# Performance work log

Measured on AMD Instinct MI355X. Metric: run time of the kernel, lower is better.

Reference implementation:

```python
import jax, jax.numpy as jnp
import numpy as np
from jax import lax
jax.config.update("jax_enable_x64", True)

B, N, H = 64, 2048, 64
FS, FC, C = 1.0e10, 3.0e11, 3.0e8
N_LAYERS, CG_STEPS = 4, 5
F32 = jnp.float32
_T64 = jnp.arange(N, dtype=jnp.float64) / FS  # time grid, float64 (FIX 7)


def _gru_dir(xproj, whh, bhh, reverse):
    # xproj: [B,N,3H] = x @ Wih^T + bih precomputed; torch gate order (r,z,n)
    def step(h, xp):
        gh = h @ whh.T + bhh
        r = jax.nn.sigmoid(xp[:, :H] + gh[:, :H])
        z = jax.nn.sigmoid(xp[:, H:2 * H] + gh[:, H:2 * H])
        n = jnp.tanh(xp[:, 2 * H:] + r * gh[:, 2 * H:])
        h2 = (1.0 - z) * n + z * h
        return h2, h2
    xs = jnp.swapaxes(xproj, 0, 1)
    if reverse:
        xs = xs[::-1]
    h0 = jnp.zeros((xproj.shape[0], H), xproj.dtype)
    _, hs = lax.scan(step, h0, xs)
    if reverse:
        hs = hs[::-1]
    return jnp.swapaxes(hs, 0, 1)


def _channel_diag(theta, bussgang_gain):
    # float64 phase: tau = R/c (single trip), phase = 2*pi*fc*(tau + (v/c)t + 0.5(a/c)t^2)
    th = theta.astype(jnp.float64)
    tau = th[:, 0:1] / C
    td = th[:, 1:2] / C
    tdd = th[:, 2:3] / C
    t = _T64[None, :]
    phase = 2.0 * np.pi * FC * (tau + td * t + 0.5 * tdd * t ** 2)
    h = jnp.exp(-1j * phase).astype(jnp.complex64)
    return h * bussgang_gain


def _forward(y_real, y_imag, theta, meta_features, gamma_eff, scale_slope, bussgang_gain,
             reg_w1, reg_b1, reg_w2, reg_b2, pw1, pb1, ln_g, ln_b, pw2, pb2, pw3, pb3,
             gru_wih_f, gru_whh_f, gru_bih_f, gru_bhh_f, gru_wih_b, gru_whh_b, gru_bih_b, gru_bhh_b,
             hw1, hb1, hw2, hb2, phase_bias):
    y_q = lax.complex(y_real, y_imag)
    # PhysicsEncoder.get_approx_fim_info
    reg = jax.nn.softplus(jax.nn.relu(gamma_eff @ reg_w1.T + reg_b1) @ reg_w2.T + reg_b2) + 1e-6  # [B,1]
    log_vol = -jnp.log(reg) * 3.0
    # PilotNavigator
    h1 = meta_features @ pw1.T + pb1
    mu = jnp.mean(h1, -1, keepdims=True)
    var = jnp.var(h1, -1, keepdims=True)
    h1 = (h1 - mu) / jnp.sqrt(var + 1e-5) * ln_g + ln_b
    h2 = jax.nn.relu(jax.nn.relu(h1) @ pw2.T + pb2)
    logits = h2 @ pw3.T + pb3
    g_PN = jax.nn.sigmoid(logits[:, 0:1])
    g_NL = jax.nn.softplus(logits[:, 1:2]) + 0.5
    physics_brake = jax.nn.sigmoid((log_vol - (-15.0)) * 5.0)
    g_grad = jax.nn.sigmoid(logits[:, 2:3]) * physics_brake
    # diagonal channel
    h_eff = _channel_diag(theta, bussgang_gain)  # [B,N] c64
    hh = (jnp.conj(h_eff) * h_eff).real  # |h|^2, [B,N]
    lam = reg  # damping from reg_net
    feats_raw = jnp.stack([y_q.real, y_q.imag], -1)  # [B,N,2]
    bias = lax.complex(jnp.cos(phase_bias), -jnp.sin(phase_bias))  # exp(-j*phase_bias)
    x_est = jnp.zeros((B, N), jnp.complex64)
    for _ in range(N_LAYERS):  # shared weights across layers
        # RiemannianPNTracker
        reliable = jnp.mean(jnp.abs(x_est)) > 0.1
        x_norm = x_est / (jnp.abs(x_est) + 1e-6)
        resid = y_q * jnp.conj(x_norm)
        feats = jnp.where(reliable, jnp.stack([resid.real, resid.imag], -1), feats_raw)
        xp_f = feats @ gru_wih_f.T + gru_bih_f
        xp_b = feats @ gru_wih_b.T + gru_bih_b
        rnn_out = jnp.concatenate([_gru_dir(xp_f, gru_whh_f, gru_bhh_f, False),
                                   _gru_dir(xp_b, gru_whh_b, gru_bhh_b, True)], axis=-1)  # [B,N,2H]
        cs = jax.nn.relu(rnn_out @ hw1.T + hb1) @ hw2.T + hb2  # [B,N,2]
        cos_p, sin_p = cs[..., 0], cs[..., 1]
        mag = jnp.sqrt(cos_p ** 2 + sin_p ** 2 + 1e-8)
        derot = lax.complex(cos_p / mag, -sin_p / mag) * bias
        eff = (1.0 - g_PN) + g_PN * derot
        eff = eff / (jnp.abs(eff) + 1e-8)
        z_in = y_q * eff
        # BussgangRefiner
        beta = scale_slope * g_NL  # [B,1]
        zr = jnp.tanh(beta * z_in.real)
        zi = jnp.tanh(beta * z_in.imag)
        z_out = lax.complex(zr, zi)
        onsager = jnp.mean(beta * (1 - zr ** 2) + beta * (1 - zi ** 2), axis=1, keepdims=True) * 0.5
        z_corr = z_out - onsager * x_est  # AMP-style Onsager correction
        # Unrolled CG: (H^H H + lam I) x = H^H z_corr, warm start x_est
        b = jnp.conj(h_eff) * z_corr
        diagA = hh + lam  # [B,N] real
        x = x_est
        r = b - diagA * x
        p = r
        rs = jnp.sum(jnp.conj(r) * r, axis=1, keepdims=True).real
        for _ in range(CG_STEPS):
            Ap = diagA * p
            alpha = rs / (jnp.sum(jnp.conj(p) * Ap, axis=1, keepdims=True).real + 1e-20)
            x = x + alpha * p
            r = r - alpha * Ap
            rs_new = jnp.sum(jnp.conj(r) * r, axis=1, keepdims=True).real
            p = r + (rs_new / (rs + 1e-20)) * p
            rs = rs_new
        x_est = (1.0 - g_grad) * x_est + g_grad * x
    return jnp.stack([x_est.real, x_est.imag], axis=-1).astype(F32)  # [B,N,2]


def setup_inputs() -> dict:
    key = jax.random.key(0)
    ks = jax.random.split(key, 20)
    def rn(k, shape, s=0.1):
        return jax.random.normal(k, shape, dtype=F32) * s
    u = jax.random.uniform(ks[0], (B, 3), dtype=F32)
    theta = jnp.stack([1e4 + u[:, 0] * 9e4, (u[:, 1] - 0.5) * 200.0, (u[:, 2] - 0.5) * 20.0], axis=1)
    return {
        "y_real": jax.random.normal(ks[1], (B, N), dtype=F32),
        "y_imag": jax.random.normal(ks[2], (B, N), dtype=F32),
        "theta": theta,
        "meta_features": jax.random.normal(ks[3], (B, 6), dtype=F32),
        "gamma_eff": jax.random.uniform(ks[4], (B, 1), dtype=F32),
        "scale_slope": jnp.asarray(1.0, F32),
        "bussgang_gain": jnp.asarray(1.0, F32),
        "reg_w1": rn(ks[5], (16, 1)), "reg_b1": jnp.zeros((16,), F32),
        "reg_w2": rn(ks[6], (1, 16)), "reg_b2": jnp.zeros((1,), F32),
        "pw1": rn(ks[7], (64, 6)), "pb1": jnp.zeros((64,), F32),
        "ln_g": jnp.ones((64,), F32), "ln_b": jnp.zeros((64,), F32),
        "pw2": rn(ks[8], (32, 64)), "pb2": jnp.zeros((32,), F32),
        "pw3": rn(ks[9], (4, 32)), "pb3": jnp.zeros((4,), F32),
        "gru_wih_f": rn(ks[10], (3 * H, 2)), "gru_whh_f": rn(ks[11], (3 * H, H)),
        "gru_bih_f": jnp.zeros((3 * H,), F32), "gru_bhh_f": jnp.zeros((3 * H,), F32),
        "gru_wih_b": rn(ks[12], (3 * H, 2)), "gru_whh_b": rn(ks[13], (3 * H, H)),
        "gru_bih_b": jnp.zeros((3 * H,), F32), "gru_bhh_b": jnp.zeros((3 * H,), F32),
        "hw1": rn(ks[14], (H // 2, 2 * H)), "hb1": jnp.zeros((H // 2,), F32),
        "hw2": rn(ks[15], (2, H // 2)), "hb2": jnp.zeros((2,), F32),
        "phase_bias": jnp.asarray(-1.5708, F32),
    }


def reference(y_real, y_imag, theta, meta_features, gamma_eff, scale_slope, bussgang_gain,
              reg_w1, reg_b1, reg_w2, reg_b2, pw1, pb1, ln_g, ln_b, pw2, pb2, pw3, pb3,
              gru_wih_f, gru_whh_f, gru_bih_f, gru_bhh_f, gru_wih_b, gru_whh_b, gru_bih_b, gru_bhh_b,
              hw1, hb1, hw2, hb2, phase_bias):
    return _forward(y_real, y_imag, theta, meta_features, gamma_eff, scale_slope, bussgang_gain,
                    reg_w1, reg_b1, reg_w2, reg_b2, pw1, pb1, ln_g, ln_b, pw2, pb2, pw3, pb3,
                    gru_wih_f, gru_whh_f, gru_bih_f, gru_bhh_f, gru_wih_b, gru_whh_b, gru_bih_b, gru_bhh_b,
                    hw1, hb1, hw2, hb2, phase_bias)
```

## Files before the change

kernel.cpp:

```cpp
#include <hip/hip_runtime.h>
#include <hip/hip_bf16.h>
#include <math.h>

#define BB 64
#define NN 2048
#define HID 64
#define NLAYERS 4
#define CGS 5

#define WS_X      0
#define WS_FEATS  (2*BB*NN)
#define WS_CS     (4*BB*NN)
#define WS_HEFF   (6*BB*NN)
#define WS_HH     (8*BB*NN)
#define WS_LAM    (9*BB*NN)
#define WS_GPN    (9*BB*NN + BB)
#define WS_GNL    (9*BB*NN + 2*BB)
#define WS_GGR    (9*BB*NN + 3*BB)
#define WS_REL    (9*BB*NN + 4*BB)
#define WS_RNN    (9*BB*NN + 4*BB + 64)

typedef float v2f __attribute__((ext_vector_type(2)));

__device__ __forceinline__ float sigf(float x) { return 1.0f / (1.0f + expf(-x)); }
__device__ __forceinline__ float softplusf(float x) {
    return fmaxf(x, 0.0f) + log1pf(expf(-fabsf(x)));
}
__device__ __forceinline__ float fsig(float x) {
    return __builtin_amdgcn_rcpf(1.0f + __expf(-x));
}
__device__ __forceinline__ float ftanh(float x) {
    float ax = fabsf(x);
    float e = __expf(-2.0f * ax);
    float t = (1.0f - e) * __builtin_amdgcn_rcpf(1.0f + e);
    return copysignf(t, x);
}

__global__ __launch_bounds__(64) void k_scalars(
    const float* __restrict__ gamma, const float* __restrict__ meta,
    const float* __restrict__ rw1, const float* __restrict__ rb1,
    const float* __restrict__ rw2, const float* __restrict__ rb2,
    const float* __restrict__ pw1, const float* __restrict__ pb1,
    const float* __restrict__ lng, const float* __restrict__ lnb,
    const float* __restrict__ pw2, const float* __restrict__ pb2,
    const float* __restrict__ pw3, const float* __restrict__ pb3,
    float* __restrict__ ws)
{
    int b = threadIdx.x;
    if (b < NLAYERS) ws[WS_REL + b] = 0.0f;
    if (b >= BB) return;

    float g = gamma[b];
    float acc = rb2[0];
    for (int j = 0; j < 16; j++) {
        float t = fmaxf(fmaf(g, rw1[j], rb1[j]), 0.0f);
        acc = fmaf(t, rw2[j], acc);
    }
    float lam = softplusf(acc) + 1e-6f;
    float log_vol = -logf(lam) * 3.0f;

    float m[6];
    for (int i = 0; i < 6; i++) m[i] = meta[b * 6 + i];
    float h1[64];
    float mu = 0.0f;
    for (int j = 0; j < 64; j++) {
        float a = pb1[j];
        for (int i = 0; i < 6; i++) a = fmaf(m[i], pw1[j * 6 + i], a);
        h1[j] = a; mu += a;
    }
    mu *= (1.0f / 64.0f);
    float var = 0.0f;
    for (int j = 0; j < 64; j++) { float d = h1[j] - mu; var = fmaf(d, d, var); }
    var *= (1.0f / 64.0f);
    float inv = 1.0f / sqrtf(var + 1e-5f);
    for (int j = 0; j < 64; j++) h1[j] = (h1[j] - mu) * inv * lng[j] + lnb[j];

    float h2[32];
    for (int k = 0; k < 32; k++) {
        float a = pb2[k];
        for (int j = 0; j < 64; j++) {
            float r = fmaxf(h1[j], 0.0f);
            a = fmaf(r, pw2[k * 64 + j], a);
        }
        h2[k] = fmaxf(a, 0.0f);
    }
    float lg[3];
    for (int o = 0; o < 3; o++) {
        float a = pb3[o];
        for (int k = 0; k < 32; k++) a = fmaf(h2[k], pw3[o * 32 + k], a);
        lg[o] = a;
    }
    float gPN = sigf(lg[0]);
    float gNL = softplusf(lg[1]) + 0.5f;
    float brake = sigf((log_vol + 15.0f) * 5.0f);
    float ggr = sigf(lg[2]) * brake;

    ws[WS_LAM + b] = lam;
    ws[WS_GPN + b] = gPN;
    ws[WS_GNL + b] = gNL;
    ws[WS_GGR + b] = ggr;
}

__global__ __launch_bounds__(256) void k_chan(
    const float* __restrict__ theta, const float* __restrict__ bg,
    float* __restrict__ ws)
{
    int idx = blockIdx.x * 256 + threadIdx.x;
    int b = idx >> 11;
    int n = idx & (NN - 1);
    double th0 = (double)theta[b * 3 + 0];
    double th1 = (double)theta[b * 3 + 1];
    double th2 = (double)theta[b * 3 + 2];
    const double Cc = 300000000.0, FS = 10000000000.0, FC = 300000000000.0;
    double tau = th0 / Cc, td = th1 / Cc, tdd = th2 / Cc;
    double t = (double)n / FS;
    double phase = 6.283185307179586 * FC * (tau + td * t + 0.5 * tdd * t * t);
    double s, c;
    sincos(phase, &s, &c);
    float gain = bg[0];
    float hr = (float)c * gain;
    float hi = (float)(-s) * gain;
    ws[WS_HEFF + 2 * idx] = hr;
    ws[WS_HEFF + 2 * idx + 1] = hi;
    ws[WS_HH + idx] = hr * hr + hi * hi;
    ws[WS_X + 2 * idx] = 0.0f;
    ws[WS_X + 2 * idx + 1] = 0.0f;
}

__global__ __launch_bounds__(256) void k_feats(
    const float* __restrict__ yr, const float* __restrict__ yi,
    float* __restrict__ ws, int layer)
{
    float rel = ws[WS_REL + layer] * (1.0f / (BB * NN));
    bool reliable = rel > 0.1f;
    int idx = blockIdx.x * 256 + threadIdx.x;
    float Yr = yr[idx], Yi = yi[idx];
    float fr, fi;
    if (reliable) {
        float xr = ws[WS_X + 2 * idx], xi = ws[WS_X + 2 * idx + 1];
        float a = sqrtf(xr * xr + xi * xi) + 1e-6f;
        float nr = xr / a, ni = xi / a;
        fr = Yr * nr + Yi * ni;
        fi = Yi * nr - Yr * ni;
    } else {
        fr = Yr; fi = Yi;
    }
    ws[WS_FEATS + 2 * idx] = fr;
    ws[WS_FEATS + 2 * idx + 1] = fi;
}

__global__ __attribute__((amdgpu_flat_work_group_size(64, 64), amdgpu_waves_per_eu(1, 1)))
void k_gru(
    const float* __restrict__ feats,
    const float* __restrict__ wih_f, const float* __restrict__ whh_f,
    const float* __restrict__ bih_f, const float* __restrict__ bhh_f,
    const float* __restrict__ wih_b, const float* __restrict__ whh_b,
    const float* __restrict__ bih_b, const float* __restrict__ bhh_b,
    float* __restrict__ rnn)
{
    __shared__ float sf[2 * NN];
    __shared__ __align__(16) float sh[HID];

    int chain = blockIdx.x;
    int b = chain >> 1;
    int d = chain & 1;
    int lane = threadIdx.x;

    const float* wih = d ? wih_b : wih_f;
    const float* whh = d ? whh_b : whh_f;
    const float* bih = d ? bih_b : bih_f;
    const float* bhh = d ? bhh_b : bhh_f;

    v2f WR[32], WZ[32], WN[32];
    {
        const float4* rr = reinterpret_cast<const float4*>(whh + (size_t)lane * 64);
        const float4* rz = reinterpret_cast<const float4*>(whh + (size_t)(64 + lane) * 64);
        const float4* rn = reinterpret_cast<const float4*>(whh + (size_t)(128 + lane) * 64);
        #pragma unroll
        for (int q = 0; q < 16; q++) {
            float4 v = rr[q]; WR[2 * q] = (v2f){v.x, v.y}; WR[2 * q + 1] = (v2f){v.z, v.w};
            float4 w = rz[q]; WZ[2 * q] = (v2f){w.x, w.y}; WZ[2 * q + 1] = (v2f){w.z, w.w};
            float4 u = rn[q]; WN[2 * q] = (v2f){u.x, u.y}; WN[2 * q + 1] = (v2f){u.z, u.w};
        }
    }
    float wir0 = wih[lane * 2],            wir1 = wih[lane * 2 + 1];
    float wiz0 = wih[(64 + lane) * 2],     wiz1 = wih[(64 + lane) * 2 + 1];
    float win0 = wih[(128 + lane) * 2],    win1 = wih[(128 + lane) * 2 + 1];
    float bir = bih[lane], biz = bih[64 + lane], bin = bih[128 + lane];
    float bhr = bhh[lane], bhz = bhh[64 + lane], bhn = bhh[128 + lane];

    {
        const float4* fp = reinterpret_cast<const float4*>(feats + (size_t)b * 2 * NN);
        float4* sp = reinterpret_cast<float4*>(sf);
        for (int j = lane; j < NN / 2; j += 64) sp[j] = fp[j];
    }
    float h = 0.0f;
    sh[lane] = 0.0f;
    __syncthreads();

    const float2* fptr = reinterpret_cast<const float2*>(sf) + (d ? (NN - 1) : 0);
    int fstep = d ? -1 : 1;
    float* optr = rnn + (size_t)b * NN * 128 + (size_t)(d ? (NN - 1) : 0) * 128
                + d * 64 + lane;
    ptrdiff_t ostep = d ? -128 : 128;

    #pragma unroll 2
    for (int s = 0; s < NN; s++) {
        float2 f = *fptr;
        fptr += fstep;
        float xpr = fmaf(f.y, wir1, fmaf(f.x, wir0, bir));
        float xpz = fmaf(f.y, wiz1, fmaf(f.x, wiz0, biz));
        float xpn = fmaf(f.y, win1, fmaf(f.x, win0, bin));

        v2f ar0 = {0, 0}, ar1 = {0, 0}, az0 = {0, 0}, az1 = {0, 0},
            an0 = {0, 0}, an1 = {0, 0};
        #pragma unroll
        for (int q = 0; q < 16; q++) {
            float4 hv = *reinterpret_cast<const float4*>(&sh[4 * q]);
            v2f h01 = {hv.x, hv.y};
            v2f h23 = {hv.z, hv.w};
            ar0 = __builtin_elementwise_fma(WR[2 * q],     h01, ar0);
            ar1 = __builtin_elementwise_fma(WR[2 * q + 1], h23, ar1);
            az0 = __builtin_elementwise_fma(WZ[2 * q],     h01, az0);
            az1 = __builtin_elementwise_fma(WZ[2 * q + 1], h23, az1);
            an0 = __builtin_elementwise_fma(WN[2 * q],     h01, an0);
            an1 = __builtin_elementwise_fma(WN[2 * q + 1], h23, an1);
        }
        float ghr = bhr + ((ar0.x + ar0.y) + (ar1.x + ar1.y));
        float ghz = bhz + ((az0.x + az0.y) + (az1.x + az1.y));
        float ghn = bhn + ((an0.x + an0.y) + (an1.x + an1.y));

        float r = fsig(xpr + ghr);
        float z = fsig(xpz + ghz);
        float n = ftanh(fmaf(r, ghn, xpn));
        h = (1.0f - z) * n + z * h;

        sh[lane] = h;
        *optr = h;
        optr += ostep;
    }
}

__global__ __launch_bounds__(256) void k_head(
    const float* __restrict__ rnn,
    const float* __restrict__ hw1, const float* __restrict__ hb1,
    const float* __restrict__ hw2, const float* __restrict__ hb2,
    float* __restrict__ cs)
{
    __shared__ float sw1[32 * 128];
    __shared__ float sb1[32], sw2[64], sb2[2];
    int tid = threadIdx.x;
    for (int i = tid; i < 4096; i += 256) sw1[i] = hw1[i];
    if (tid < 32) sb1[tid] = hb1[tid];
    if (tid < 64) sw2[tid] = hw2[tid];
    if (tid < 2)  sb2[tid] = hb2[tid];
    __syncthreads();

    int idx = blockIdx.x * 256 + tid;
    float x[128];
    const float4* rp = reinterpret_cast<const float4*>(rnn + (size_t)idx * 128);
    #pragma unroll
    for (int q = 0; q < 32; q++) {
        float4 v = rp[q];
        x[q * 4 + 0] = v.x;
        x[q * 4 + 1] = v.y;
        x[q * 4 + 2] = v.z;
        x[q * 4 + 3] = v.w;
    }

    float c0 = sb2[0], c1 = sb2[1];
    for (int k = 0; k < 32; k++) {
        float a = sb1[k];
        #pragma unroll
        for (int j = 0; j < 128; j++) a = fmaf(x[j], sw1[k * 128 + j], a);
        a = fmaxf(a, 0.0f);
        c0 = fmaf(a, sw2[k], c0);
        c1 = fmaf(a, sw2[32 + k], c1);
    }
    cs[2 * idx] = c0;
    cs[2 * idx + 1] = c1;
}

__device__ __forceinline__ float block_sum(float v, float* sred, int tid) {
    #pragma unroll
    for (int o = 32; o > 0; o >>= 1) v += __shfl_down(v, o, 64);
    __syncthreads();
    if ((tid & 63) == 0) sred[tid >> 6] = v;
    __syncthreads();
    return sred[0] + sred[1] + sred[2] + sred[3];
}

__global__ __launch_bounds__(256) void k_solve(
    const float* __restrict__ yr, const float* __restrict__ yi,
    float* __restrict__ ws,
    const float* __restrict__ scale_slope, const float* __restrict__ phase_bias,
    float* __restrict__ out, int layer)
{
    __shared__ float sred[4];
    int b = blockIdx.x, tid = threadIdx.x;
    float lam = ws[WS_LAM + b], gPN = ws[WS_GPN + b];
    float gNL = ws[WS_GNL + b], gg = ws[WS_GGR + b];
    float beta = scale_slope[0] * gNL;
    float pb = phase_bias[0];
    float bsr = cosf(pb), bsi = -sinf(pb);

    float Yr[8], Yi[8], Hr[8], Hi[8], dA[8], Xr[8], Xi[8], Br[8], Bi[8];
    float ons = 0.0f;
    #pragma unroll
    for (int i = 0; i < 8; i++) {
        int idx = b * NN + tid + i * 256;
        float yr_ = yr[idx], yi_ = yi[idx];
        float c = ws[WS_CS + 2 * idx], s = ws[WS_CS + 2 * idx + 1];
        float mag = sqrtf(c * c + s * s + 1e-8f);
        float dr = c / mag, di = -s / mag;
        float der = dr * bsr - di * bsi;
        float dei = dr * bsi + di * bsr;
        float er = 1.0f - gPN + gPN * der;
        float ei = gPN * dei;
        float ea = sqrtf(er * er + ei * ei) + 1e-8f;
        er /= ea; ei /= ea;
        float zri = yr_ * er - yi_ * ei;
        float zii = yr_ * ei + yi_ * er;
        float zr = tanhf(beta * zri);
        float zi = tanhf(beta * zii);
        ons += beta * (1.0f - zr * zr) + beta * (1.0f - zi * zi);
        Yr[i] = yr_; Yi[i] = yi_;
        Hr[i] = ws[WS_HEFF + 2 * idx]; Hi[i] = ws[WS_HEFF + 2 * idx + 1];
        dA[i] = ws[WS_HH + idx] + lam;
        Xr[i] = ws[WS_X + 2 * idx]; Xi[i] = ws[WS_X + 2 * idx + 1];
        Br[i] = zr; Bi[i] = zi;
    }
    float onsager = block_sum(ons, sred, tid) * (0.5f / NN);

    #pragma unroll
    for (int i = 0; i < 8; i++) {
        float zcr = Br[i] - onsager * Xr[i];
        float zci = Bi[i] - onsager * Xi[i];
        Br[i] = Hr[i] * zcr + Hi[i] * zci;
        Bi[i] = Hr[i] * zci - Hi[i] * zcr;
    }

    float xr[8], xi[8], Rr[8], Ri[8], Pr[8], Pi[8];
    float rs_p = 0.0f;
    #pragma unroll
    for (int i = 0; i < 8; i++) {
        xr[i] = Xr[i]; xi[i] = Xi[i];
        Rr[i] = Br[i] - dA[i] * xr[i];
        Ri[i] = Bi[i] - dA[i] * xi[i];
        Pr[i] = Rr[i]; Pi[i] = Ri[i];
        rs_p += Rr[i] * Rr[i] + Ri[i] * Ri[i];
    }
    float rs = block_sum(rs_p, sred, tid);

    for (int it = 0; it < CGS; it++) {
        float pap = 0.0f;
        #pragma unroll
        for (int i = 0; i < 8; i++) pap += dA[i] * (Pr[i] * Pr[i] + Pi[i] * Pi[i]);
        float alpha = rs / (block_sum(pap, sred, tid) + 1e-20f);
        float rsn_p = 0.0f;
        #pragma unroll
        for (int i = 0; i < 8; i++) {
            xr[i] += alpha * Pr[i]; xi[i] += alpha * Pi[i];
            Rr[i] -= alpha * dA[i] * Pr[i];
            Ri[i] -= alpha * dA[i] * Pi[i];
            rsn_p += Rr[i] * Rr[i] + Ri[i] * Ri[i];
        }
        float rsn = block_sum(rsn_p, sred, tid);
        float bsc = rsn / (rs + 1e-20f);
        #pragma unroll
        for (int i = 0; i < 8; i++) {
            Pr[i] = Rr[i] + bsc * Pr[i];
            Pi[i] = Ri[i] + bsc * Pi[i];
        }
        rs = rsn;
    }

    float relp = 0.0f;
    float* dstx = (layer == NLAYERS - 1) ? out : (ws + WS_X);
    #pragma unroll
    for (int i = 0; i < 8; i++) {
        int idx = b * NN + tid + i * 256;
        float nr = (1.0f - gg) * Xr[i] + gg * xr[i];
        float ni = (1.0f - gg) * Xi[i] + gg * xi[i];
        dstx[2 * idx] = nr;
        dstx[2 * idx + 1] = ni;
        if (layer < NLAYERS - 1) {
            ws[WS_X + 2 * idx] = nr;
            ws[WS_X + 2 * idx + 1] = ni;
        }
        relp += sqrtf(nr * nr + ni * ni);
    }
    float relsum = block_sum(relp, sred, tid);
    if (tid == 0 && layer + 1 < NLAYERS) atomicAdd(ws + WS_REL + layer + 1, relsum);
}

extern "C" void kernel_launch(void* const* d_in, const int* in_sizes, int n_in,
                              void* d_out, int out_size, void* d_ws, size_t ws_size,
                              hipStream_t stream)
{
    const float* yr    = (const float*)d_in[0];
    const float* yi    = (const float*)d_in[1];
    const float* theta = (const float*)d_in[2];
    const float* meta  = (const float*)d_in[3];
    const float* gamma = (const float*)d_in[4];
    const float* sslope= (const float*)d_in[5];
    const float* bgain = (const float*)d_in[6];
    const float* rw1   = (const float*)d_in[7];
    const float* rb1   = (const float*)d_in[8];
    const float* rw2   = (const float*)d_in[9];
    const float* rb2   = (const float*)d_in[10];
    const float* pw1   = (const float*)d_in[11];
    const float* pb1   = (const float*)d_in[12];
    const float* lng   = (const float*)d_in[13];
    const float* lnb   = (const float*)d_in[14];
    const float* pw2   = (const float*)d_in[15];
    const float* pb2   = (const float*)d_in[16];
    const float* pw3   = (const float*)d_in[17];
    const float* pb3   = (const float*)d_in[18];
    const float* wih_f = (const float*)d_in[19];
    const float* whh_f = (const float*)d_in[20];
    const float* bih_f = (const float*)d_in[21];
    const float* bhh_f = (const float*)d_in[22];
    const float* wih_b = (const float*)d_in[23];
    const float* whh_b = (const float*)d_in[24];
    const float* bih_b = (const float*)d_in[25];
    const float* bhh_b = (const float*)d_in[26];
    const float* hw1   = (const float*)d_in[27];
    const float* hb1   = (const float*)d_in[28];
    const float* hw2   = (const float*)d_in[29];
    const float* hb2   = (const float*)d_in[30];
    const float* pbias = (const float*)d_in[31];

    float* ws = (float*)d_ws;
    float* out = (float*)d_out;
    float* rnn = ws + WS_RNN;

    k_scalars<<<1, 64, 0, stream>>>(gamma, meta, rw1, rb1, rw2, rb2,
                                    pw1, pb1, lng, lnb, pw2, pb2, pw3, pb3, ws);
    k_chan<<<(BB * NN) / 256, 256, 0, stream>>>(theta, bgain, ws);

    for (int L = 0; L < NLAYERS; L++) {
        k_feats<<<(BB * NN) / 256, 256, 0, stream>>>(yr, yi, ws, L);
        k_gru<<<BB * 2, 64, 0, stream>>>(ws + WS_FEATS,
                                         wih_f, whh_f, bih_f, bhh_f,
                                         wih_b, whh_b, bih_b, bhh_b, rnn);
        k_head<<<(BB * NN) / 256, 256, 0, stream>>>(rnn, hw1, hb1, hw2, hb2,
                                                    ws + WS_CS);
        k_solve<<<BB, 256, 0, stream>>>(yr, yi, ws, sslope, pbias, out, L);
    }
}
```

Before: 3.315 ms.

## Split GRU recurrent matvec across four waves with LDS partial-sum reduction

The GRU kernel grows from one wave to four waves per chain. Each wave handles a quarter of the hidden-state inputs to the recurrent matvec, so it holds a quarter of the weights in registers. Partial gate sums go through double-buffered LDS and are combined after a workgroup barrier at every timestep. Each wave then redundantly computes the full h update, keeping only its own slice for the next step. This shortens the serial FMA chain per step, at the cost of a barrier and extra LDS traffic each step.

```diff
diff --git a/kernel.cpp b/kernel.cpp
--- a/kernel.cpp
+++ b/kernel.cpp
@@ -149,8 +149,7 @@
     ws[WS_FEATS + 2 * idx + 1] = fi;
 }
 
-__global__ __attribute__((amdgpu_flat_work_group_size(64, 64), amdgpu_waves_per_eu(1, 1)))
-void k_gru(
+__global__ __launch_bounds__(256) void k_gru(
     const float* __restrict__ feats,
     const float* __restrict__ wih_f, const float* __restrict__ whh_f,
     const float* __restrict__ bih_f, const float* __restrict__ bhh_f,
@@ -159,28 +158,31 @@
     float* __restrict__ rnn)
 {
     __shared__ float sf[2 * NN];
-    __shared__ __align__(16) float sh[HID];
+    __shared__ __align__(16) float shq[4][16];
+    __shared__ float P[2][3][4][64];
 
     int chain = blockIdx.x;
     int b = chain >> 1;
     int d = chain & 1;
-    int lane = threadIdx.x;
+    int tid = threadIdx.x;
+    int lane = tid & 63;
+    int w = tid >> 6;
 
     const float* wih = d ? wih_b : wih_f;
     const float* whh = d ? whh_b : whh_f;
     const float* bih = d ? bih_b : bih_f;
     const float* bhh = d ? bhh_b : bhh_f;
 
-    v2f WR[32], WZ[32], WN[32];
+    v2f WR[8], WZ[8], WN[8];
     {
-        const float4* rr = reinterpret_cast<const float4*>(whh + (size_t)lane * 64);
-        const float4* rz = reinterpret_cast<const float4*>(whh + (size_t)(64 + lane) * 64);
-        const float4* rn = reinterpret_cast<const float4*>(whh + (size_t)(128 + lane) * 64);
-        #pragma unroll
-        for (int q = 0; q < 16; q++) {
+        const float4* rr = reinterpret_cast<const float4*>(whh + (size_t)lane * 64 + 16 * w);
+        const float4* rz = reinterpret_cast<const float4*>(whh + (size_t)(64 + lane) * 64 + 16 * w);
+        const float4* rn = reinterpret_cast<const float4*>(whh + (size_t)(128 + lane) * 64 + 16 * w);
+        #pragma unroll
+        for (int q = 0; q < 4; q++) {
             float4 v = rr[q]; WR[2 * q] = (v2f){v.x, v.y}; WR[2 * q + 1] = (v2f){v.z, v.w};
-            float4 w = rz[q]; WZ[2 * q] = (v2f){w.x, w.y}; WZ[2 * q + 1] = (v2f){w.z, w.w};
-            float4 u = rn[q]; WN[2 * q] = (v2f){u.x, u.y}; WN[2 * q + 1] = (v2f){u.z, u.w};
+            float4 u = rz[q]; WZ[2 * q] = (v2f){u.x, u.y}; WZ[2 * q + 1] = (v2f){u.z, u.w};
+            float4 x = rn[q]; WN[2 * q] = (v2f){x.x, x.y}; WN[2 * q + 1] = (v2f){x.z, x.w};
         }
     }
     float wir0 = wih[lane * 2],            wir1 = wih[lane * 2 + 1];
@@ -192,10 +194,10 @@
     {
         const float4* fp = reinterpret_cast<const float4*>(feats + (size_t)b * 2 * NN);
         float4* sp = reinterpret_cast<float4*>(sf);
-        for (int j = lane; j < NN / 2; j += 64) sp[j] = fp[j];
+        for (int j = tid; j < NN / 2; j += 256) sp[j] = fp[j];
     }
     float h = 0.0f;
-    sh[lane] = 0.0f;
+    if ((lane >> 4) == w) shq[w][lane & 15] = 0.0f;
     __syncthreads();
 
     const float2* fptr = reinterpret_cast<const float2*>(sf) + (d ? (NN - 1) : 0);
@@ -206,6 +208,7 @@
 
     #pragma unroll 2
     for (int s = 0; s < NN; s++) {
+        int pb = s & 1;
         float2 f = *fptr;
         fptr += fstep;
         float xpr = fmaf(f.y, wir1, fmaf(f.x, wir0, bir));
@@ -215,8 +218,8 @@
         v2f ar0 = {0, 0}, ar1 = {0, 0}, az0 = {0, 0}, az1 = {0, 0},
             an0 = {0, 0}, an1 = {0, 0};
         #pragma unroll
-        for (int q = 0; q < 16; q++) {
-            float4 hv = *reinterpret_cast<const float4*>(&sh[4 * q]);
+        for (int q = 0; q < 4; q++) {
+            float4 hv = *reinterpret_cast<const float4*>(&shq[w][4 * q]);
             v2f h01 = {hv.x, hv.y};
             v2f h23 = {hv.z, hv.w};
             ar0 = __builtin_elementwise_fma(WR[2 * q],     h01, ar0);
@@ -226,17 +229,29 @@
             an0 = __builtin_elementwise_fma(WN[2 * q],     h01, an0);
             an1 = __builtin_elementwise_fma(WN[2 * q + 1], h23, an1);
         }
-        float ghr = bhr + ((ar0.x + ar0.y) + (ar1.x + ar1.y));
-        float ghz = bhz + ((az0.x + az0.y) + (az1.x + az1.y));
-        float ghn = bhn + ((an0.x + an0.y) + (an1.x + an1.y));
+        v2f ars = ar0 + ar1, azs = az0 + az1, ans = an0 + an1;
+        P[pb][0][w][lane] = ars.x + ars.y;
+        P[pb][1][w][lane] = azs.x + azs.y;
+        P[pb][2][w][lane] = ans.x + ans.y;
+
+        asm volatile("s_waitcnt lgkmcnt(0)" ::: "memory");
+        __builtin_amdgcn_s_barrier();
+        asm volatile("" ::: "memory");
+
+        float ghr = bhr + ((P[pb][0][0][lane] + P[pb][0][1][lane]) +
+                           (P[pb][0][2][lane] + P[pb][0][3][lane]));
+        float ghz = bhz + ((P[pb][1][0][lane] + P[pb][1][1][lane]) +
+                           (P[pb][1][2][lane] + P[pb][1][3][lane]));
+        float ghn = bhn + ((P[pb][2][0][lane] + P[pb][2][1][lane]) +
+                           (P[pb][2][2][lane] + P[pb][2][3][lane]));
 
         float r = fsig(xpr + ghr);
         float z = fsig(xpz + ghz);
         float n = ftanh(fmaf(r, ghn, xpn));
         h = (1.0f - z) * n + z * h;
 
-        sh[lane] = h;
-        *optr = h;
+        if ((lane >> 4) == w) shq[w][lane & 15] = h;
+        if (w == 0) *optr = h;
         optr += ostep;
     }
 }
@@ -441,9 +456,9 @@
 
     for (int L = 0; L < NLAYERS; L++) {
         k_feats<<<(BB * NN) / 256, 256, 0, stream>>>(yr, yi, ws, L);
-        k_gru<<<BB * 2, 64, 0, stream>>>(ws + WS_FEATS,
-                                         wih_f, whh_f, bih_f, bhh_f,
-                                         wih_b, whh_b, bih_b, bhh_b, rnn);
+        k_gru<<<BB * 2, 256, 0, stream>>>(ws + WS_FEATS,
+                                          wih_f, whh_f, bih_f, bhh_f,
+                                          wih_b, whh_b, bih_b, bhh_b, rnn);
         k_head<<<(BB * NN) / 256, 256, 0, stream>>>(rnn, hw1, hb1, hw2, hb2,
                                                     ws + WS_CS);
         k_solve<<<BB, 256, 0, stream>>>(yr, yi, ws, sslope, pbias, out, L);
```

Measured after the change: 3.287 ms. No clear change (-0.8%).

## Process two batch chains per GRU block to share register-resident weights

Applied to the files above, without the earlier changes.

Each GRU workgroup now runs two batch elements for the same direction at once, halving the grid from 128 to 64 blocks. Both chains reuse the same register-held Whh weights, and their independent dependency chains are interleaved to hide latency in the serial recurrence. The cost is double the per-step work for each wave and half as many active CUs, so the sequential critical path per block grows. It pays off only if instruction-level overlap outweighs the extra work.

```diff
diff --git a/kernel.cpp b/kernel.cpp
--- a/kernel.cpp
+++ b/kernel.cpp
@@ -158,12 +158,13 @@
     const float* __restrict__ bih_b, const float* __restrict__ bhh_b,
     float* __restrict__ rnn)
 {
-    __shared__ float sf[2 * NN];
-    __shared__ __align__(16) float sh[HID];
-
-    int chain = blockIdx.x;
-    int b = chain >> 1;
-    int d = chain & 1;
+    __shared__ float sfA[2 * NN], sfB[2 * NN];
+    __shared__ __align__(16) float shA[HID], shB[HID];
+
+    int bp = blockIdx.x;
+    int d = bp & 1;
+    int p = bp >> 1;
+    int b0 = 2 * p, b1 = 2 * p + 1;
     int lane = threadIdx.x;
 
     const float* wih = d ? wih_b : wih_f;
@@ -190,54 +191,82 @@
     float bhr = bhh[lane], bhz = bhh[64 + lane], bhn = bhh[128 + lane];
 
     {
-        const float4* fp = reinterpret_cast<const float4*>(feats + (size_t)b * 2 * NN);
-        float4* sp = reinterpret_cast<float4*>(sf);
-        for (int j = lane; j < NN / 2; j += 64) sp[j] = fp[j];
-    }
-    float h = 0.0f;
-    sh[lane] = 0.0f;
+        const float4* fpA = reinterpret_cast<const float4*>(feats + (size_t)b0 * 2 * NN);
+        const float4* fpB = reinterpret_cast<const float4*>(feats + (size_t)b1 * 2 * NN);
+        float4* spA = reinterpret_cast<float4*>(sfA);
+        float4* spB = reinterpret_cast<float4*>(sfB);
+        for (int j = lane; j < NN / 2; j += 64) { spA[j] = fpA[j]; spB[j] = fpB[j]; }
+    }
+    float hA = 0.0f, hB = 0.0f;
+    shA[lane] = 0.0f;
+    shB[lane] = 0.0f;
     __syncthreads();
 
-    const float2* fptr = reinterpret_cast<const float2*>(sf) + (d ? (NN - 1) : 0);
+    const float2* fptrA = reinterpret_cast<const float2*>(sfA) + (d ? (NN - 1) : 0);
+    const float2* fptrB = reinterpret_cast<const float2*>(sfB) + (d ? (NN - 1) : 0);
     int fstep = d ? -1 : 1;
-    float* optr = rnn + (size_t)b * NN * 128 + (size_t)(d ? (NN - 1) : 0) * 128
-                + d * 64 + lane;
+    size_t o0 = (size_t)(d ? (NN - 1) : 0) * 128 + d * 64 + lane;
+    float* optrA = rnn + (size_t)b0 * NN * 128 + o0;
+    float* optrB = rnn + (size_t)b1 * NN * 128 + o0;
     ptrdiff_t ostep = d ? -128 : 128;
 
     #pragma unroll 2
     for (int s = 0; s < NN; s++) {
-        float2 f = *fptr;
-        fptr += fstep;
-        float xpr = fmaf(f.y, wir1, fmaf(f.x, wir0, bir));
-        float xpz = fmaf(f.y, wiz1, fmaf(f.x, wiz0, biz));
-        float xpn = fmaf(f.y, win1, fmaf(f.x, win0, bin));
-
-        v2f ar0 = {0, 0}, ar1 = {0, 0}, az0 = {0, 0}, az1 = {0, 0},
-            an0 = {0, 0}, an1 = {0, 0};
+        float2 fA = *fptrA; fptrA += fstep;
+        float2 fB = *fptrB; fptrB += fstep;
+        float xprA = fmaf(fA.y, wir1, fmaf(fA.x, wir0, bir));
+        float xpzA = fmaf(fA.y, wiz1, fmaf(fA.x, wiz0, biz));
+        float xpnA = fmaf(fA.y, win1, fmaf(fA.x, win0, bin));
+        float xprB = fmaf(fB.y, wir1, fmaf(fB.x, wir0, bir));
+        float xpzB = fmaf(fB.y, wiz1, fmaf(fB.x, wiz0, biz));
+        float xpnB = fmaf(fB.y, win1, fmaf(fB.x, win0, bin));
+
+        v2f arA0 = {0,0}, arA1 = {0,0}, azA0 = {0,0}, azA1 = {0,0}, anA0 = {0,0}, anA1 = {0,0};
+        v2f arB0 = {0,0}, arB1 = {0,0}, azB0 = {0,0}, azB1 = {0,0}, anB0 = {0,0}, anB1 = {0,0};
         #pragma unroll
         for (int q = 0; q < 16; q++) {
-            float4 hv = *reinterpret_cast<const float4*>(&sh[4 * q]);
-            v2f h01 = {hv.x, hv.y};
-            v2f h23 = {hv.z, hv.w};
-            ar0 = __builtin_elementwise_fma(WR[2 * q],     h01, ar0);
-            ar1 = __builtin_elementwise_fma(WR[2 * q + 1], h23, ar1);
-            az0 = __builtin_elementwise_fma(WZ[2 * q],     h01, az0);
-            az1 = __builtin_elementwise_fma(WZ[2 * q + 1], h23, az1);
-            an0 = __builtin_elementwise_fma(WN[2 * q],     h01, an0);
-            an1 = __builtin_elementwise_fma(WN[2 * q + 1], h23, an1);
-        }
-        float ghr = bhr + ((ar0.x + ar0.y) + (ar1.x + ar1.y));
-        float ghz = bhz + ((az0.x + az0.y) + (az1.x + az1.y));
-        float ghn = bhn + ((an0.x + an0.y) + (an1.x + an1.y));
-
-        float r = fsig(xpr + ghr);
-        float z = fsig(xpz + ghz);
-        float n = ftanh(fmaf(r, ghn, xpn));
-        h = (1.0f - z) * n + z * h;
-
-        sh[lane] = h;
-        *optr = h;
-        optr += ostep;
+            float4 hvA = *reinterpret_cast<const float4*>(&shA[4 * q]);
+            float4 hvB = *reinterpret_cast<const float4*>(&shB[4 * q]);
+            v2f hA01 = {hvA.x, hvA.y}, hA23 = {hvA.z, hvA.w};
+            v2f hB01 = {hvB.x, hvB.y}, hB23 = {hvB.z, hvB.w};
+            v2f wr0 = WR[2 * q], wr1 = WR[2 * q + 1];
+            v2f wz0 = WZ[2 * q], wz1 = WZ[2 * q + 1];
+            v2f wn0 = WN[2 * q], wn1 = WN[2 * q + 1];
+            arA0 = __builtin_elementwise_fma(wr0, hA01, arA0);
+            arB0 = __builtin_elementwise_fma(wr0, hB01, arB0);
+            arA1 = __builtin_elementwise_fma(wr1, hA23, arA1);
+            arB1 = __builtin_elementwise_fma(wr1, hB23, arB1);
+            azA0 = __builtin_elementwise_fma(wz0, hA01, azA0);
+            azB0 = __builtin_elementwise_fma(wz0, hB01, azB0);
+            azA1 = __builtin_elementwise_fma(wz1, hA23, azA1);
+            azB1 = __builtin_elementwise_fma(wz1, hB23, azB1);
+            anA0 = __builtin_elementwise_fma(wn0, hA01, anA0);
+            anB0 = __builtin_elementwise_fma(wn0, hB01, anB0);
+            anA1 = __builtin_elementwise_fma(wn1, hA23, anA1);
+            anB1 = __builtin_elementwise_fma(wn1, hB23, anB1);
+        }
+        v2f arsA = arA0 + arA1, azsA = azA0 + azA1, ansA = anA0 + anA1;
+        v2f arsB = arB0 + arB1, azsB = azB0 + azB1, ansB = anB0 + anB1;
+        float ghrA = bhr + (arsA.x + arsA.y);
+        float ghzA = bhz + (azsA.x + azsA.y);
+        float ghnA = bhn + (ansA.x + ansA.y);
+        float ghrB = bhr + (arsB.x + arsB.y);
+        float ghzB = bhz + (azsB.x + azsB.y);
+        float ghnB = bhn + (ansB.x + ansB.y);
+
+        float rA = fsig(xprA + ghrA);
+        float rB = fsig(xprB + ghrB);
+        float zA = fsig(xpzA + ghzA);
+        float zB = fsig(xpzB + ghzB);
+        float nA = ftanh(fmaf(rA, ghnA, xpnA));
+        float nB = ftanh(fmaf(rB, ghnB, xpnB));
+        hA = (1.0f - zA) * nA + zA * hA;
+        hB = (1.0f - zB) * nB + zB * hB;
+
+        shA[lane] = hA;
+        shB[lane] = hB;
+        *optrA = hA; optrA += ostep;
+        *optrB = hB; optrB += ostep;
     }
 }
 
@@ -441,9 +470,9 @@
 
     for (int L = 0; L < NLAYERS; L++) {
         k_feats<<<(BB * NN) / 256, 256, 0, stream>>>(yr, yi, ws, L);
-        k_gru<<<BB * 2, 64, 0, stream>>>(ws + WS_FEATS,
-                                         wih_f, whh_f, bih_f, bhh_f,
-                                         wih_b, whh_b, bih_b, bhh_b, rnn);
+        k_gru<<<64, 64, 0, stream>>>(ws + WS_FEATS,
+                                     wih_f, whh_f, bih_f, bhh_f,
+                                     wih_b, whh_b, bih_b, bhh_b, rnn);
         k_head<<<(BB * NN) / 256, 256, 0, stream>>>(rnn, hw1, hb1, hw2, hb2,
                                                     ws + WS_CS);
         k_solve<<<BB, 256, 0, stream>>>(yr, yi, ws, sslope, pbias, out, L);
```

New measurement: 10.54 ms. 3.18x slower.
